# Kernel tuning notes

Measured on AMD Instinct MI355X. Metric: run time of the kernel, lower is better.

## Reference

```python
import jax, jax.numpy as jnp
import numpy as np

N_NODES = 50000
N_EDGES = 800000
D_IN = 128
D_OUT = 128


def setup_inputs() -> dict:
    key = jax.random.key(0)
    ks = jax.random.split(key, 10)
    x = jax.random.normal(ks[0], (N_NODES, D_IN), dtype=jnp.float32)
    src = jax.random.randint(ks[1], (N_EDGES,), 0, N_NODES, dtype=jnp.int32)
    dst = jax.random.randint(ks[2], (N_EDGES,), 0, N_NODES, dtype=jnp.int32)
    s = 1.0 / np.sqrt(D_IN)
    def lin(k, din, dout):
        kw, kb = jax.random.split(k)
        W = jax.random.uniform(kw, (din, dout), minval=-s, maxval=s, dtype=jnp.float32)
        b = jax.random.uniform(kb, (dout,), minval=-s, maxval=s, dtype=jnp.float32)
        return W, b
    W1, b1 = lin(ks[3], D_IN, D_IN)
    W2, b2 = lin(ks[4], D_IN, D_IN)
    W3, b3 = lin(ks[5], D_IN, D_OUT)
    return dict(x=x, W1=W1, b1=b1, W2=W2, b2=b2, W3=W3, b3=b3, src=src, dst=dst)


def reference(x, W1, b1, W2, b2, W3, b3, src, dst):
    n = x.shape[0]
    ones = jnp.ones(src.shape[0], dtype=x.dtype)
    in_deg = jax.ops.segment_sum(ones, dst, num_segments=n)    # [N]
    out_deg = jax.ops.segment_sum(ones, src, num_segments=n)   # [N]

    def sage_gcn(h, W, b):
        # DGL SAGEConv(aggregator_type='gcn'), eval mode (feat_drop = identity):
        # h_neigh = (sum_{j in N(i)} h_j + h_i) / (in_deg_i + 1); out = h_neigh @ W + b
        neigh = jax.ops.segment_sum(h[src], dst, num_segments=n)  # [N, D]
        h_neigh = (neigh + h) / (in_deg + 1.0)[:, None]
        return h_neigh @ W + b

    h = sage_gcn(x, W1, b1)
    h = sage_gcn(h, W2, b2)

    # DGL GraphConv norm='both', allow_zero_in_degree=True:
    # out = D_in^{-1/2} A D_out^{-1/2} h W + b, degrees clamped to >= 1
    norm_out = jnp.clip(out_deg, 1.0) ** -0.5
    norm_in = jnp.clip(in_deg, 1.0) ** -0.5
    hs = h * norm_out[:, None]
    agg = jax.ops.segment_sum(hs[src], dst, num_segments=n)
    out = (agg * norm_in[:, None]) @ W3 + b3
    return out
```

## Files before the change

kernel.cpp:

```cpp
#include <hip/hip_runtime.h>

#define NN 50000
#define NE 800000
#define D 128

#define CH 32
#define EPC (NE / CH)
#define RGH 4
#define NPRH (NN / RGH)
#define CSRCAP (NE + 16 * NN)

#define HIST_BLOCKS (CH * RGH)
#define CVT_BLOCKS 1563
#define WT_BLOCKS 48

typedef short bf16x8 __attribute__((ext_vector_type(8)));
typedef float f32x4 __attribute__((ext_vector_type(4)));


__device__ __forceinline__ unsigned bf16rne(float f) {
  unsigned u = __float_as_uint(f);
  return (u + 0x7fffu + ((u >> 16) & 1u)) >> 16;
}
__device__ __forceinline__ unsigned packbf(float lo, float hi) {
  return bf16rne(lo) | (bf16rne(hi) << 16);
}

__global__ __launch_bounds__(1024) void cvtw_hist_kernel(
    const float* __restrict__ x, const float* __restrict__ W1,
    const float* __restrict__ W2, const float* __restrict__ W3,
    unsigned short* __restrict__ hbf, unsigned short* __restrict__ T1,
    unsigned short* __restrict__ T2, unsigned short* __restrict__ T3,
    const int* __restrict__ src, const int* __restrict__ dst,
    int* __restrict__ partial_dst, int* __restrict__ partial_src) {
  __shared__ int hd[NPRH];
  __shared__ int hs[NPRH];
  int b = blockIdx.x;
  int tid = threadIdx.x;
  if (b < HIST_BLOCKS) {
    int c = b >> 2;
    int r = b & 3;
    int base = r * NPRH;
    for (int i = tid; i < NPRH; i += 1024) { hd[i] = 0; hs[i] = 0; }
    __syncthreads();
    int e0 = c * EPC;
    for (int i = tid; i < EPC; i += 1024) {
      int d = dst[e0 + i];
      int s = src[e0 + i];
      unsigned dr = (unsigned)(d - base);
      unsigned sr = (unsigned)(s - base);
      if (dr < NPRH) atomicAdd(&hd[dr], 1);
      if (sr < NPRH) atomicAdd(&hs[sr], 1);
    }
    __syncthreads();
    for (int i = tid; i < NPRH; i += 1024) {
      partial_dst[c * NN + base + i] = hd[i];
      partial_src[c * NN + base + i] = hs[i];
    }
  } else if (b < HIST_BLOCKS + CVT_BLOCKS) {
    int i = (b - HIST_BLOCKS) * 1024 + tid;
    if (i < NN * D / 4) {
      float4 v = ((const float4*)x)[i];
      uint2 p;
      p.x = packbf(v.x, v.y);
      p.y = packbf(v.z, v.w);
      ((uint2*)hbf)[i] = p;
    }
  } else if (b < HIST_BLOCKS + CVT_BLOCKS + WT_BLOCKS) {
    int g = b - (HIST_BLOCKS + CVT_BLOCKS);
    int w = g >> 4;
    int i = (g & 15) * 1024 + tid;
    const float* W = (w == 0) ? W1 : (w == 1) ? W2 : W3;
    unsigned short* T = (w == 0) ? T1 : (w == 1) ? T2 : T3;
    int n = i >> 7, k = i & 127;
    T[n * 128 + k] = (unsigned short)bf16rne(W[k * 128 + n]);
  } else {
    if (tid < 16) ((uint4*)(hbf + (size_t)NN * D))[tid] = make_uint4(0, 0, 0, 0);
  }
}

__device__ __forceinline__ int block_excl_scan(int v, int* wsum) {
  int lane = threadIdx.x & 63;
  int w = threadIdx.x >> 6;
  int incl = v;
#pragma unroll
  for (int off = 1; off < 64; off <<= 1) {
    int t = __shfl_up(incl, off);
    if (lane >= off) incl += t;
  }
  if (lane == 63) wsum[w] = incl;
  __syncthreads();
  int wo = 0;
#pragma unroll
  for (int j = 0; j < 4; ++j)
    if (j < w) wo += wsum[j];
  return wo + incl - v;
}

__global__ __launch_bounds__(256) void degscan_kernel(int* __restrict__ partial_dst,
                                                      const int* __restrict__ partial_src,
                                                      int* __restrict__ degtmp,
                                                      int* __restrict__ deg_out,
                                                      int* __restrict__ row_ptr,
                                                      int* __restrict__ partials, int N) {
  __shared__ int wsum[4];
  int d = blockIdx.x * 256 + threadIdx.x;
  int run = 0;
  if (d < N) {
#pragma unroll
    for (int c = 0; c < CH; ++c) {
      int v = partial_dst[c * NN + d];
      partial_dst[c * NN + d] = run;
      run += v;
    }
    degtmp[d] = run;
    int ro = 0;
#pragma unroll
    for (int c = 0; c < CH; ++c) ro += partial_src[c * NN + d];
    deg_out[d] = ro;
  }
  int pad = (run + 3) & ~3;
  int excl = block_excl_scan(pad, wsum);
  if (d <= N) row_ptr[d] = excl;
  if (threadIdx.x == 255) partials[blockIdx.x] = excl + pad;
}

__global__ __launch_bounds__(256) void scan2(int* __restrict__ partials, int nb) {
  __shared__ int wsum[4];
  int v = (threadIdx.x < nb) ? partials[threadIdx.x] : 0;
  int excl = block_excl_scan(v, wsum);
  if (threadIdx.x < nb) partials[threadIdx.x] = excl;
}

__global__ __launch_bounds__(1024) void fill_kernel(const int* __restrict__ src,
                                                    const int* __restrict__ dst,
                                                    const int* __restrict__ row_ptr,
                                                    const int* __restrict__ partials,
                                                    const int* __restrict__ partial_dst,
                                                    int* __restrict__ csr_src) {
  __shared__ int cur[NPRH];
  int tid = threadIdx.x;
  int c = blockIdx.x >> 2;
  int r = blockIdx.x & 3;
  int base = r * NPRH;
  for (int i = tid; i < NPRH; i += 1024) {
    int nd = base + i;
    cur[i] = row_ptr[nd] + partials[nd >> 8] + partial_dst[c * NN + nd];
  }
  __syncthreads();
  int e0 = c * EPC;
  for (int i = tid; i < EPC; i += 1024) {
    int d = dst[e0 + i];
    unsigned dr = (unsigned)(d - base);
    if (dr < NPRH) {
      int pos = atomicAdd(&cur[dr], 1);
      csr_src[pos] = src[e0 + i];
    }
  }
  if (c == CH - 1) {
    __syncthreads();
    for (int i = tid; i < NPRH; i += 1024) {
      int nd = base + i;
      int s = cur[i];
      int e = row_ptr[nd + 1] + partials[(nd + 1) >> 8];
      for (int j = s; j < e; ++j) csr_src[j] = NN;
    }
  }
}

__device__ __forceinline__ void bacc(float* a, uint4 u) {
  a[0] += __uint_as_float(u.x << 16);
  a[1] += __uint_as_float(u.x & 0xffff0000u);
  a[2] += __uint_as_float(u.y << 16);
  a[3] += __uint_as_float(u.y & 0xffff0000u);
  a[4] += __uint_as_float(u.z << 16);
  a[5] += __uint_as_float(u.z & 0xffff0000u);
  a[6] += __uint_as_float(u.w << 16);
  a[7] += __uint_as_float(u.w & 0xffff0000u);
}

template <int MODE>
__global__ __launch_bounds__(256, 8) void agg_kernel(const unsigned short* __restrict__ hb,
                                                     const int* __restrict__ row_ptr,
                                                     const int* __restrict__ partials,
                                                     const int* __restrict__ csr_src,
                                                     const int* __restrict__ degtmp,
                                                     unsigned short* __restrict__ outb, int N) {
  int qw = threadIdx.x >> 4;
  int col = threadIdx.x & 15;
  int node = blockIdx.x * 16 + qw;
  if (node >= N) return;
  int start = row_ptr[node] + partials[node >> 8];
  int end = row_ptr[node + 1] + partials[(node + 1) >> 8];
  int indeg = degtmp[node];
  uint4 srow = make_uint4(0, 0, 0, 0);
  if (MODE == 0) srow = ((const uint4*)(hb + (size_t)node * D))[col];
  float a0[8] = {0, 0, 0, 0, 0, 0, 0, 0};
  float a1[8] = {0, 0, 0, 0, 0, 0, 0, 0};
  const int* ce = csr_src + start;
  int cnt = end - start;
  for (int it = 0; it < cnt; it += 4) {
    int4 ix = *(const int4*)(ce + it);
    uint4 u0 = ((const uint4*)(hb + (size_t)ix.x * D))[col];
    uint4 u1 = ((const uint4*)(hb + (size_t)ix.y * D))[col];
    uint4 u2 = ((const uint4*)(hb + (size_t)ix.z * D))[col];
    uint4 u3 = ((const uint4*)(hb + (size_t)ix.w * D))[col];
    bacc(a0, u0);
    bacc(a1, u1);
    bacc(a0, u2);
    bacc(a1, u3);
  }
#pragma unroll
  for (int j = 0; j < 8; ++j) a0[j] += a1[j];
  if (MODE == 0) {
    float sf[8] = {0, 0, 0, 0, 0, 0, 0, 0};
    bacc(sf, srow);
    float inv = 1.0f / (float)(indeg + 1);
#pragma unroll
    for (int j = 0; j < 8; ++j) a0[j] = (a0[j] + sf[j]) * inv;
  } else {
    float sc = rsqrtf(fmaxf((float)indeg, 1.0f));
#pragma unroll
    for (int j = 0; j < 8; ++j) a0[j] *= sc;
  }
  uint4 p;
  p.x = packbf(a0[0], a0[1]);
  p.y = packbf(a0[2], a0[3]);
  p.z = packbf(a0[4], a0[5]);
  p.w = packbf(a0[6], a0[7]);
  ((uint4*)(outb + (size_t)node * D))[col] = p;
}

template <int MODE, int OUT_BF>
__global__ __launch_bounds__(256) void mgemm_kernel(const unsigned short* __restrict__ A,
                                                    const unsigned short* __restrict__ WT,
                                                    const float* __restrict__ bias,
                                                    const int* __restrict__ deg_out,
                                                    float* __restrict__ outf,
                                                    unsigned short* __restrict__ outb, int N) {
  __shared__ unsigned short sWT[128 * 136];
  int tid = threadIdx.x;
  for (int g = tid; g < 2048; g += 256) {
    int n = g >> 4, c = g & 15;
    uint4 v = ((const uint4*)WT)[g];
    *(uint4*)&sWT[n * 136 + c * 8] = v;
  }
  int wv = tid >> 6;
  int lane = tid & 63;
  int q = lane >> 4;
  int ln = lane & 15;
  int row0 = blockIdx.x * 64 + wv * 16;
  int arow = row0 + ln;
  if (arow >= N) arow = 0;
  const unsigned short* Ar = A + (size_t)arow * 128 + q * 8;
  bf16x8 af0 = *(const bf16x8*)(Ar + 0);
  bf16x8 af1 = *(const bf16x8*)(Ar + 32);
  bf16x8 af2 = *(const bf16x8*)(Ar + 64);
  bf16x8 af3 = *(const bf16x8*)(Ar + 96);
  f32x4 acc[8];
#pragma unroll
  for (int t = 0; t < 8; ++t) acc[t] = (f32x4){0.f, 0.f, 0.f, 0.f};
  __syncthreads();
#pragma unroll
  for (int t = 0; t < 8; ++t) {
    const unsigned short* Wr = &sWT[(t * 16 + ln) * 136 + q * 8];
    bf16x8 b0 = *(const bf16x8*)(Wr + 0);
    bf16x8 b1 = *(const bf16x8*)(Wr + 32);
    bf16x8 b2 = *(const bf16x8*)(Wr + 64);
    bf16x8 b3 = *(const bf16x8*)(Wr + 96);
    acc[t] = __builtin_amdgcn_mfma_f32_16x16x32_bf16(af0, b0, acc[t], 0, 0, 0);
    acc[t] = __builtin_amdgcn_mfma_f32_16x16x32_bf16(af1, b1, acc[t], 0, 0, 0);
    acc[t] = __builtin_amdgcn_mfma_f32_16x16x32_bf16(af2, b2, acc[t], 0, 0, 0);
    acc[t] = __builtin_amdgcn_mfma_f32_16x16x32_bf16(af3, b3, acc[t], 0, 0, 0);
  }
  float scl[4];
#pragma unroll
  for (int r = 0; r < 4; ++r) {
    scl[r] = 1.0f;
    if (MODE == 1) {
      int row = row0 + q * 4 + r;
      int rr = (row < N) ? row : 0;
      scl[r] = rsqrtf(fmaxf((float)deg_out[rr], 1.0f));
    }
  }
#pragma unroll
  for (int t = 0; t < 8; ++t) {
    float b = bias[t * 16 + ln];
#pragma unroll
    for (int r = 0; r < 4; ++r) {
      int row = row0 + q * 4 + r;
      if (row < N) {
        float v = (acc[t][r] + b) * scl[r];
        if (OUT_BF)
          outb[(size_t)row * 128 + t * 16 + ln] = (unsigned short)bf16rne(v);
        else
          outf[(size_t)row * 128 + t * 16 + ln] = v;
      }
    }
  }
}


extern "C" void kernel_launch(void* const* d_in, const int* in_sizes, int n_in,
                              void* d_out, int out_size, void* d_ws, size_t ws_size,
                              hipStream_t stream) {
  const float* x = (const float*)d_in[0];
  const float* W1 = (const float*)d_in[1];
  const float* b1 = (const float*)d_in[2];
  const float* W2 = (const float*)d_in[3];
  const float* b2 = (const float*)d_in[4];
  const float* W3 = (const float*)d_in[5];
  const float* b3 = (const float*)d_in[6];
  const int* src = (const int*)d_in[7];
  const int* dst = (const int*)d_in[8];
  float* out = (float*)d_out;

  const int N = NN;

  unsigned short* hbf = (unsigned short*)d_ws;
  unsigned short* aggB = hbf + (size_t)(NN + 1) * D;
  unsigned short* WT1 = aggB + (size_t)NN * D;
  unsigned short* WT2 = WT1 + D * D;
  unsigned short* WT3 = WT2 + D * D;
  int* partial_dst = (int*)(WT3 + D * D);
  int* partial_src = partial_dst + (size_t)CH * NN;
  int* degtmp = partial_src + (size_t)CH * NN;
  int* deg_out = degtmp + NN;
  int* row_ptr = deg_out + NN;
  int* partials = row_ptr + NN + 1;
  int* csr_src = partials + 256;

  const int scanBlocks = (N + 255) / 256;

  cvtw_hist_kernel<<<HIST_BLOCKS + CVT_BLOCKS + WT_BLOCKS + 1, 1024, 0, stream>>>(
      x, W1, W2, W3, hbf, WT1, WT2, WT3, src, dst, partial_dst, partial_src);
  degscan_kernel<<<scanBlocks, 256, 0, stream>>>(partial_dst, partial_src, degtmp,
                                                 deg_out, row_ptr, partials, N);
  scan2<<<1, 256, 0, stream>>>(partials, scanBlocks);
  fill_kernel<<<CH * RGH, 1024, 0, stream>>>(src, dst, row_ptr, partials, partial_dst,
                                             csr_src);

  int aggBlocks = (N + 15) / 16;
  int gemmBlocks = (N + 63) / 64;

  agg_kernel<0><<<aggBlocks, 256, 0, stream>>>(hbf, row_ptr, partials, csr_src, degtmp,
                                               aggB, N);
  mgemm_kernel<0, 1><<<gemmBlocks, 256, 0, stream>>>(aggB, WT1, b1, deg_out, nullptr, hbf, N);
  agg_kernel<0><<<aggBlocks, 256, 0, stream>>>(hbf, row_ptr, partials, csr_src, degtmp,
                                               aggB, N);
  mgemm_kernel<1, 1><<<gemmBlocks, 256, 0, stream>>>(aggB, WT2, b2, deg_out, nullptr, hbf, N);
  agg_kernel<1><<<aggBlocks, 256, 0, stream>>>(hbf, row_ptr, partials, csr_src, degtmp,
                                               aggB, N);
  mgemm_kernel<0, 0><<<gemmBlocks, 256, 0, stream>>>(aggB, WT3, b3, deg_out, out, nullptr, N);
}
```

Before: 260.9 us.

## Fuse aggregation with GEMM per layer and simplify CSR build with global atomics

```diff
diff --git a/kernel.cpp b/kernel.cpp
--- a/kernel.cpp
+++ b/kernel.cpp
@@ -4,15 +4,10 @@
 #define NE 800000
 #define D 128
 
-#define CH 32
-#define EPC (NE / CH)
-#define RGH 4
-#define NPRH (NN / RGH)
-#define CSRCAP (NE + 16 * NN)
-
-#define HIST_BLOCKS (CH * RGH)
+#define HISTB 800
 #define CVT_BLOCKS 1563
 #define WT_BLOCKS 48
+#define CSRCAP (NE + 4 * NN)
 
 typedef short bf16x8 __attribute__((ext_vector_type(8)));
 typedef float f32x4 __attribute__((ext_vector_type(4)));
@@ -25,149 +20,6 @@
 __device__ __forceinline__ unsigned packbf(float lo, float hi) {
   return bf16rne(lo) | (bf16rne(hi) << 16);
 }
-
-__global__ __launch_bounds__(1024) void cvtw_hist_kernel(
-    const float* __restrict__ x, const float* __restrict__ W1,
-    const float* __restrict__ W2, const float* __restrict__ W3,
-    unsigned short* __restrict__ hbf, unsigned short* __restrict__ T1,
-    unsigned short* __restrict__ T2, unsigned short* __restrict__ T3,
-    const int* __restrict__ src, const int* __restrict__ dst,
-    int* __restrict__ partial_dst, int* __restrict__ partial_src) {
-  __shared__ int hd[NPRH];
-  __shared__ int hs[NPRH];
-  int b = blockIdx.x;
-  int tid = threadIdx.x;
-  if (b < HIST_BLOCKS) {
-    int c = b >> 2;
-    int r = b & 3;
-    int base = r * NPRH;
-    for (int i = tid; i < NPRH; i += 1024) { hd[i] = 0; hs[i] = 0; }
-    __syncthreads();
-    int e0 = c * EPC;
-    for (int i = tid; i < EPC; i += 1024) {
-      int d = dst[e0 + i];
-      int s = src[e0 + i];
-      unsigned dr = (unsigned)(d - base);
-      unsigned sr = (unsigned)(s - base);
-      if (dr < NPRH) atomicAdd(&hd[dr], 1);
-      if (sr < NPRH) atomicAdd(&hs[sr], 1);
-    }
-    __syncthreads();
-    for (int i = tid; i < NPRH; i += 1024) {
-      partial_dst[c * NN + base + i] = hd[i];
-      partial_src[c * NN + base + i] = hs[i];
-    }
-  } else if (b < HIST_BLOCKS + CVT_BLOCKS) {
-    int i = (b - HIST_BLOCKS) * 1024 + tid;
-    if (i < NN * D / 4) {
-      float4 v = ((const float4*)x)[i];
-      uint2 p;
-      p.x = packbf(v.x, v.y);
-      p.y = packbf(v.z, v.w);
-      ((uint2*)hbf)[i] = p;
-    }
-  } else if (b < HIST_BLOCKS + CVT_BLOCKS + WT_BLOCKS) {
-    int g = b - (HIST_BLOCKS + CVT_BLOCKS);
-    int w = g >> 4;
-    int i = (g & 15) * 1024 + tid;
-    const float* W = (w == 0) ? W1 : (w == 1) ? W2 : W3;
-    unsigned short* T = (w == 0) ? T1 : (w == 1) ? T2 : T3;
-    int n = i >> 7, k = i & 127;
-    T[n * 128 + k] = (unsigned short)bf16rne(W[k * 128 + n]);
-  } else {
-    if (tid < 16) ((uint4*)(hbf + (size_t)NN * D))[tid] = make_uint4(0, 0, 0, 0);
-  }
-}
-
-__device__ __forceinline__ int block_excl_scan(int v, int* wsum) {
-  int lane = threadIdx.x & 63;
-  int w = threadIdx.x >> 6;
-  int incl = v;
-#pragma unroll
-  for (int off = 1; off < 64; off <<= 1) {
-    int t = __shfl_up(incl, off);
-    if (lane >= off) incl += t;
-  }
-  if (lane == 63) wsum[w] = incl;
-  __syncthreads();
-  int wo = 0;
-#pragma unroll
-  for (int j = 0; j < 4; ++j)
-    if (j < w) wo += wsum[j];
-  return wo + incl - v;
-}
-
-__global__ __launch_bounds__(256) void degscan_kernel(int* __restrict__ partial_dst,
-                                                      const int* __restrict__ partial_src,
-                                                      int* __restrict__ degtmp,
-                                                      int* __restrict__ deg_out,
-                                                      int* __restrict__ row_ptr,
-                                                      int* __restrict__ partials, int N) {
-  __shared__ int wsum[4];
-  int d = blockIdx.x * 256 + threadIdx.x;
-  int run = 0;
-  if (d < N) {
-#pragma unroll
-    for (int c = 0; c < CH; ++c) {
-      int v = partial_dst[c * NN + d];
-      partial_dst[c * NN + d] = run;
-      run += v;
-    }
-    degtmp[d] = run;
-    int ro = 0;
-#pragma unroll
-    for (int c = 0; c < CH; ++c) ro += partial_src[c * NN + d];
-    deg_out[d] = ro;
-  }
-  int pad = (run + 3) & ~3;
-  int excl = block_excl_scan(pad, wsum);
-  if (d <= N) row_ptr[d] = excl;
-  if (threadIdx.x == 255) partials[blockIdx.x] = excl + pad;
-}
-
-__global__ __launch_bounds__(256) void scan2(int* __restrict__ partials, int nb) {
-  __shared__ int wsum[4];
-  int v = (threadIdx.x < nb) ? partials[threadIdx.x] : 0;
-  int excl = block_excl_scan(v, wsum);
-  if (threadIdx.x < nb) partials[threadIdx.x] = excl;
-}
-
-__global__ __launch_bounds__(1024) void fill_kernel(const int* __restrict__ src,
-                                                    const int* __restrict__ dst,
-                                                    const int* __restrict__ row_ptr,
-                                                    const int* __restrict__ partials,
-                                                    const int* __restrict__ partial_dst,
-                                                    int* __restrict__ csr_src) {
-  __shared__ int cur[NPRH];
-  int tid = threadIdx.x;
-  int c = blockIdx.x >> 2;
-  int r = blockIdx.x & 3;
-  int base = r * NPRH;
-  for (int i = tid; i < NPRH; i += 1024) {
-    int nd = base + i;
-    cur[i] = row_ptr[nd] + partials[nd >> 8] + partial_dst[c * NN + nd];
-  }
-  __syncthreads();
-  int e0 = c * EPC;
-  for (int i = tid; i < EPC; i += 1024) {
-    int d = dst[e0 + i];
-    unsigned dr = (unsigned)(d - base);
-    if (dr < NPRH) {
-      int pos = atomicAdd(&cur[dr], 1);
-      csr_src[pos] = src[e0 + i];
-    }
-  }
-  if (c == CH - 1) {
-    __syncthreads();
-    for (int i = tid; i < NPRH; i += 1024) {
-      int nd = base + i;
-      int s = cur[i];
-      int e = row_ptr[nd + 1] + partials[(nd + 1) >> 8];
-      for (int j = s; j < e; ++j) csr_src[j] = NN;
-    }
-  }
-}
-
 __device__ __forceinline__ void bacc(float* a, uint4 u) {
   a[0] += __uint_as_float(u.x << 16);
   a[1] += __uint_as_float(u.x & 0xffff0000u);
@@ -179,80 +31,180 @@
   a[7] += __uint_as_float(u.w & 0xffff0000u);
 }
 
-template <int MODE>
-__global__ __launch_bounds__(256, 8) void agg_kernel(const unsigned short* __restrict__ hb,
-                                                     const int* __restrict__ row_ptr,
+__global__ __launch_bounds__(1024) void prep_kernel(
+    const float* __restrict__ x, const float* __restrict__ W1,
+    const float* __restrict__ W2, const float* __restrict__ W3,
+    const int* __restrict__ src, const int* __restrict__ dst,
+    unsigned short* __restrict__ h0, unsigned short* __restrict__ h1,
+    unsigned short* __restrict__ T1, unsigned short* __restrict__ T2,
+    unsigned short* __restrict__ T3, int* __restrict__ deg_in,
+    int* __restrict__ deg_out) {
+  int b = blockIdx.x;
+  int tid = threadIdx.x;
+  if (b < HISTB) {
+    int i = b * 1024 + tid;
+    if (i < NE) {
+      atomicAdd(&deg_in[dst[i]], 1);
+      atomicAdd(&deg_out[src[i]], 1);
+    }
+  } else if (b < HISTB + CVT_BLOCKS) {
+    int i = (b - HISTB) * 1024 + tid;
+    if (i < NN * D / 4) {
+      float4 v = ((const float4*)x)[i];
+      uint2 p;
+      p.x = packbf(v.x, v.y);
+      p.y = packbf(v.z, v.w);
+      ((uint2*)h0)[i] = p;
+    }
+  } else if (b < HISTB + CVT_BLOCKS + WT_BLOCKS) {
+    int g = b - (HISTB + CVT_BLOCKS);
+    int w = g >> 4;
+    int i = (g & 15) * 1024 + tid;
+    const float* W = (w == 0) ? W1 : (w == 1) ? W2 : W3;
+    unsigned short* T = (w == 0) ? T1 : (w == 1) ? T2 : T3;
+    int n = i >> 7, k = i & 127;
+    T[n * 128 + k] = (unsigned short)bf16rne(W[k * 128 + n]);
+  } else {
+    if (tid < 16) {
+      ((uint4*)(h0 + (size_t)NN * D))[tid] = make_uint4(0, 0, 0, 0);
+      ((uint4*)(h1 + (size_t)NN * D))[tid] = make_uint4(0, 0, 0, 0);
+    }
+  }
+}
+
+__device__ __forceinline__ int block_excl_scan(int v, int* wsum) {
+  int lane = threadIdx.x & 63;
+  int w = threadIdx.x >> 6;
+  int incl = v;
+#pragma unroll
+  for (int off = 1; off < 64; off <<= 1) {
+    int t = __shfl_up(incl, off);
+    if (lane >= off) incl += t;
+  }
+  if (lane == 63) wsum[w] = incl;
+  __syncthreads();
+  int wo = 0;
+#pragma unroll
+  for (int j = 0; j < 4; ++j)
+    if (j < w) wo += wsum[j];
+  return wo + incl - v;
+}
+
+__global__ __launch_bounds__(256) void degscan_kernel(const int* __restrict__ deg_in,
+                                                      int* __restrict__ row_ptr,
+                                                      int* __restrict__ partials, int N) {
+  __shared__ int wsum[4];
+  int d = blockIdx.x * 256 + threadIdx.x;
+  int run = (d < N) ? deg_in[d] : 0;
+  int pad = (run + 3) & ~3;
+  int excl = block_excl_scan(pad, wsum);
+  if (d <= N) row_ptr[d] = excl;
+  if (threadIdx.x == 255) partials[blockIdx.x] = excl + pad;
+}
+
+__global__ __launch_bounds__(256) void scan2(int* __restrict__ partials, int nb) {
+  __shared__ int wsum[4];
+  int v = (threadIdx.x < nb) ? partials[threadIdx.x] : 0;
+  int excl = block_excl_scan(v, wsum);
+  if (threadIdx.x < nb) partials[threadIdx.x] = excl;
+}
+
+__global__ __launch_bounds__(256) void curpad_kernel(const int* __restrict__ row_ptr,
                                                      const int* __restrict__ partials,
-                                                     const int* __restrict__ csr_src,
-                                                     const int* __restrict__ degtmp,
-                                                     unsigned short* __restrict__ outb, int N) {
-  int qw = threadIdx.x >> 4;
-  int col = threadIdx.x & 15;
-  int node = blockIdx.x * 16 + qw;
-  if (node >= N) return;
-  int start = row_ptr[node] + partials[node >> 8];
-  int end = row_ptr[node + 1] + partials[(node + 1) >> 8];
-  int indeg = degtmp[node];
-  uint4 srow = make_uint4(0, 0, 0, 0);
-  if (MODE == 0) srow = ((const uint4*)(hb + (size_t)node * D))[col];
-  float a0[8] = {0, 0, 0, 0, 0, 0, 0, 0};
-  float a1[8] = {0, 0, 0, 0, 0, 0, 0, 0};
-  const int* ce = csr_src + start;
-  int cnt = end - start;
-  for (int it = 0; it < cnt; it += 4) {
-    int4 ix = *(const int4*)(ce + it);
-    uint4 u0 = ((const uint4*)(hb + (size_t)ix.x * D))[col];
-    uint4 u1 = ((const uint4*)(hb + (size_t)ix.y * D))[col];
-    uint4 u2 = ((const uint4*)(hb + (size_t)ix.z * D))[col];
-    uint4 u3 = ((const uint4*)(hb + (size_t)ix.w * D))[col];
-    bacc(a0, u0);
-    bacc(a1, u1);
-    bacc(a0, u2);
-    bacc(a1, u3);
-  }
-#pragma unroll
-  for (int j = 0; j < 8; ++j) a0[j] += a1[j];
-  if (MODE == 0) {
-    float sf[8] = {0, 0, 0, 0, 0, 0, 0, 0};
-    bacc(sf, srow);
-    float inv = 1.0f / (float)(indeg + 1);
-#pragma unroll
-    for (int j = 0; j < 8; ++j) a0[j] = (a0[j] + sf[j]) * inv;
-  } else {
-    float sc = rsqrtf(fmaxf((float)indeg, 1.0f));
-#pragma unroll
-    for (int j = 0; j < 8; ++j) a0[j] *= sc;
-  }
-  uint4 p;
-  p.x = packbf(a0[0], a0[1]);
-  p.y = packbf(a0[2], a0[3]);
-  p.z = packbf(a0[4], a0[5]);
-  p.w = packbf(a0[6], a0[7]);
-  ((uint4*)(outb + (size_t)node * D))[col] = p;
-}
-
-template <int MODE, int OUT_BF>
-__global__ __launch_bounds__(256) void mgemm_kernel(const unsigned short* __restrict__ A,
-                                                    const unsigned short* __restrict__ WT,
-                                                    const float* __restrict__ bias,
-                                                    const int* __restrict__ deg_out,
-                                                    float* __restrict__ outf,
-                                                    unsigned short* __restrict__ outb, int N) {
+                                                     const int* __restrict__ deg_in,
+                                                     int* __restrict__ cur,
+                                                     int* __restrict__ csr_src, int N) {
+  int i = blockIdx.x * 256 + threadIdx.x;
+  if (i >= N) return;
+  int st = row_ptr[i] + partials[i >> 8];
+  int en = row_ptr[i + 1] + partials[(i + 1) >> 8];
+  cur[i] = st;
+  int deg = deg_in[i];
+  for (int j = st + deg; j < en; ++j) csr_src[j] = NN;
+}
+
+__global__ __launch_bounds__(1024) void fill_kernel(const int* __restrict__ src,
+                                                    const int* __restrict__ dst,
+                                                    int* __restrict__ cur,
+                                                    int* __restrict__ csr_src) {
+  int i = blockIdx.x * 1024 + threadIdx.x;
+  if (i < NE) {
+    int d = dst[i];
+    int pos = atomicAdd(&cur[d], 1);
+    csr_src[pos] = src[i];
+  }
+}
+
+template <int MODE_AGG, int MODE_SCALE, int OUT_BF>
+__global__ __launch_bounds__(256) void fused_kernel(
+    const unsigned short* __restrict__ tin, const int* __restrict__ row_ptr,
+    const int* __restrict__ partials, const int* __restrict__ csr_src,
+    const int* __restrict__ deg_in, const int* __restrict__ deg_out,
+    const unsigned short* __restrict__ WT, const float* __restrict__ bias,
+    unsigned short* __restrict__ outb, float* __restrict__ outf, int N) {
   __shared__ unsigned short sWT[128 * 136];
+  __shared__ unsigned short sA[64 * 136];
   int tid = threadIdx.x;
   for (int g = tid; g < 2048; g += 256) {
     int n = g >> 4, c = g & 15;
     uint4 v = ((const uint4*)WT)[g];
     *(uint4*)&sWT[n * 136 + c * 8] = v;
   }
+  int qw = tid >> 4;
+  int col = tid & 15;
+  int nb = blockIdx.x * 64;
+#pragma unroll 1
+  for (int s = 0; s < 4; ++s) {
+    int nl = qw * 4 + s;
+    int node = nb + nl;
+    float a0[8] = {0, 0, 0, 0, 0, 0, 0, 0};
+    float a1[8] = {0, 0, 0, 0, 0, 0, 0, 0};
+    if (node < N) {
+      int start = row_ptr[node] + partials[node >> 8];
+      int end = row_ptr[node + 1] + partials[(node + 1) >> 8];
+      int indeg = deg_in[node];
+      uint4 srow = make_uint4(0, 0, 0, 0);
+      if (MODE_AGG == 0) srow = ((const uint4*)(tin + (size_t)node * D))[col];
+      const int* ce = csr_src + start;
+      int cnt = end - start;
+      for (int it = 0; it < cnt; it += 4) {
+        int4 ix = *(const int4*)(ce + it);
+        uint4 u0 = ((const uint4*)(tin + (size_t)ix.x * D))[col];
+        uint4 u1 = ((const uint4*)(tin + (size_t)ix.y * D))[col];
+        uint4 u2 = ((const uint4*)(tin + (size_t)ix.z * D))[col];
+        uint4 u3 = ((const uint4*)(tin + (size_t)ix.w * D))[col];
+        bacc(a0, u0);
+        bacc(a1, u1);
+        bacc(a0, u2);
+        bacc(a1, u3);
+      }
+#pragma unroll
+      for (int j = 0; j < 8; ++j) a0[j] += a1[j];
+      if (MODE_AGG == 0) {
+        float sf[8] = {0, 0, 0, 0, 0, 0, 0, 0};
+        bacc(sf, srow);
+        float inv = 1.0f / (float)(indeg + 1);
+#pragma unroll
+        for (int j = 0; j < 8; ++j) a0[j] = (a0[j] + sf[j]) * inv;
+      } else {
+        float sc = rsqrtf(fmaxf((float)indeg, 1.0f));
+#pragma unroll
+        for (int j = 0; j < 8; ++j) a0[j] *= sc;
+      }
+    }
+    uint4 p;
+    p.x = packbf(a0[0], a0[1]);
+    p.y = packbf(a0[2], a0[3]);
+    p.z = packbf(a0[4], a0[5]);
+    p.w = packbf(a0[6], a0[7]);
+    *(uint4*)&sA[nl * 136 + col * 8] = p;
+  }
+  __syncthreads();
   int wv = tid >> 6;
   int lane = tid & 63;
   int q = lane >> 4;
   int ln = lane & 15;
-  int row0 = blockIdx.x * 64 + wv * 16;
-  int arow = row0 + ln;
-  if (arow >= N) arow = 0;
-  const unsigned short* Ar = A + (size_t)arow * 128 + q * 8;
+  const unsigned short* Ar = &sA[(wv * 16 + ln) * 136 + q * 8];
   bf16x8 af0 = *(const bf16x8*)(Ar + 0);
   bf16x8 af1 = *(const bf16x8*)(Ar + 32);
   bf16x8 af2 = *(const bf16x8*)(Ar + 64);
@@ -260,7 +212,6 @@
   f32x4 acc[8];
 #pragma unroll
   for (int t = 0; t < 8; ++t) acc[t] = (f32x4){0.f, 0.f, 0.f, 0.f};
-  __syncthreads();
 #pragma unroll
   for (int t = 0; t < 8; ++t) {
     const unsigned short* Wr = &sWT[(t * 16 + ln) * 136 + q * 8];
@@ -277,8 +228,8 @@
 #pragma unroll
   for (int r = 0; r < 4; ++r) {
     scl[r] = 1.0f;
-    if (MODE == 1) {
-      int row = row0 + q * 4 + r;
+    if (MODE_SCALE == 1) {
+      int row = nb + wv * 16 + q * 4 + r;
       int rr = (row < N) ? row : 0;
       scl[r] = rsqrtf(fmaxf((float)deg_out[rr], 1.0f));
     }
@@ -288,7 +239,7 @@
     float b = bias[t * 16 + ln];
 #pragma unroll
     for (int r = 0; r < 4; ++r) {
-      int row = row0 + q * 4 + r;
+      int row = nb + wv * 16 + q * 4 + r;
       if (row < N) {
         float v = (acc[t][r] + b) * scl[r];
         if (OUT_BF)
@@ -317,39 +268,35 @@
 
   const int N = NN;
 
-  unsigned short* hbf = (unsigned short*)d_ws;
-  unsigned short* aggB = hbf + (size_t)(NN + 1) * D;
-  unsigned short* WT1 = aggB + (size_t)NN * D;
+  unsigned short* h0 = (unsigned short*)d_ws;
+  unsigned short* h1 = h0 + (size_t)(NN + 1) * D;
+  unsigned short* WT1 = h1 + (size_t)(NN + 1) * D;
   unsigned short* WT2 = WT1 + D * D;
   unsigned short* WT3 = WT2 + D * D;
-  int* partial_dst = (int*)(WT3 + D * D);
-  int* partial_src = partial_dst + (size_t)CH * NN;
-  int* degtmp = partial_src + (size_t)CH * NN;
-  int* deg_out = degtmp + NN;
+  int* deg_in = (int*)(WT3 + D * D);
+  int* deg_out = deg_in + NN;
   int* row_ptr = deg_out + NN;
-  int* partials = row_ptr + NN + 1;
-  int* csr_src = partials + 256;
+  int* partials = row_ptr + NN + 4;
+  int* cur = partials + 256;
+  int* csr_src = cur + NN;
 
   const int scanBlocks = (N + 255) / 256;
 
-  cvtw_hist_kernel<<<HIST_BLOCKS + CVT_BLOCKS + WT_BLOCKS + 1, 1024, 0, stream>>>(
-      x, W1, W2, W3, hbf, WT1, WT2, WT3, src, dst, partial_dst, partial_src);
-  degscan_kernel<<<scanBlocks, 256, 0, stream>>>(partial_dst, partial_src, degtmp,
-                                                 deg_out, row_ptr, partials, N);
+  hipMemsetAsync(deg_in, 0, 2 * (size_t)NN * sizeof(int), stream);
+  prep_kernel<<<HISTB + CVT_BLOCKS + WT_BLOCKS + 1, 1024, 0, stream>>>(
+      x, W1, W2, W3, src, dst, h0, h1, WT1, WT2, WT3, deg_in, deg_out);
+  degscan_kernel<<<scanBlocks, 256, 0, stream>>>(deg_in, row_ptr, partials, N);
   scan2<<<1, 256, 0, stream>>>(partials, scanBlocks);
-  fill_kernel<<<CH * RGH, 1024, 0, stream>>>(src, dst, row_ptr, partials, partial_dst,
-                                             csr_src);
-
-  int aggBlocks = (N + 15) / 16;
-  int gemmBlocks = (N + 63) / 64;
-
-  agg_kernel<0><<<aggBlocks, 256, 0, stream>>>(hbf, row_ptr, partials, csr_src, degtmp,
-                                               aggB, N);
-  mgemm_kernel<0, 1><<<gemmBlocks, 256, 0, stream>>>(aggB, WT1, b1, deg_out, nullptr, hbf, N);
-  agg_kernel<0><<<aggBlocks, 256, 0, stream>>>(hbf, row_ptr, partials, csr_src, degtmp,
-                                               aggB, N);
-  mgemm_kernel<1, 1><<<gemmBlocks, 256, 0, stream>>>(aggB, WT2, b2, deg_out, nullptr, hbf, N);
-  agg_kernel<1><<<aggBlocks, 256, 0, stream>>>(hbf, row_ptr, partials, csr_src, degtmp,
-                                               aggB, N);
-  mgemm_kernel<0, 0><<<gemmBlocks, 256, 0, stream>>>(aggB, WT3, b3, deg_out, out, nullptr, N);
-}
+  curpad_kernel<<<scanBlocks, 256, 0, stream>>>(row_ptr, partials, deg_in, cur,
+                                                csr_src, N);
+  fill_kernel<<<HISTB, 1024, 0, stream>>>(src, dst, cur, csr_src);
+
+  int layerBlocks = (N + 63) / 64;
+
+  fused_kernel<0, 0, 1><<<layerBlocks, 256, 0, stream>>>(
+      h0, row_ptr, partials, csr_src, deg_in, deg_out, WT1, b1, h1, nullptr, N);
+  fused_kernel<0, 1, 1><<<layerBlocks, 256, 0, stream>>>(
+      h1, row_ptr, partials, csr_src, deg_in, deg_out, WT2, b2, h0, nullptr, N);
+  fused_kernel<1, 0, 0><<<layerBlocks, 256, 0, stream>>>(
+      h0, row_ptr, partials, csr_src, deg_in, deg_out, WT3, b3, nullptr, out, N);
+}
```

New measurement: 370.8 us. 1.42x slower.
